# Optimization experiments

Hardware: AMD Instinct MI355X
Metric: run time of the kernel (lower is better)

## Reference

```python
import jax, jax.numpy as jnp
import numpy as np
from jax.scipy.special import logsumexp

B, S, E, H = 32, 1024, 512, 256  # batch, seq_len, sent_emb_dim, per-direction lstm hidden
NT, NTB = 16, 5
PAD, SOS, EOS = 0, 1, 2
NEG = -1000000.0


def _lstm(x, h0, c0, wih, whh, bih, bhh):
    # x: [B,S,I] -> outputs [B,S,H]; torch gate order i,f,g,o
    def step(carry, xt):
        h, c = carry
        z = xt @ wih.T + h @ whh.T + bih + bhh
        i, f, g, o = jnp.split(z, 4, axis=-1)
        c = jax.nn.sigmoid(f) * c + jax.nn.sigmoid(i) * jnp.tanh(g)
        h = jax.nn.sigmoid(o) * jnp.tanh(c)
        return (h, c), h
    _, hs = jax.lax.scan(step, (h0, c0), jnp.swapaxes(x, 0, 1))
    return jnp.swapaxes(hs, 0, 1)


def _bilstm(x, h0, c0, pf, pb):
    fwd = _lstm(x, h0[0], c0[0], *pf)
    bwd = _lstm(x[:, ::-1], h0[1], c0[1], *pb)[:, ::-1]
    return jnp.concatenate([fwd, bwd], axis=-1)  # [B,S,2H]


def _crf_nll(emissions, tags, mask, T):
    # gold-path score
    first = T[SOS, tags[:, 0]] + jnp.take_along_axis(emissions[:, 0], tags[:, 0:1], axis=1)[:, 0]
    e = jnp.take_along_axis(emissions, tags[:, :, None], axis=2)[:, :, 0]        # [B,S]
    tr = T[tags[:, :-1], tags[:, 1:]]                                            # [B,S-1]
    scores = first + jnp.sum((e[:, 1:] + tr) * mask[:, 1:], axis=1)
    last_idx = mask.sum(1).astype(jnp.int32) - 1
    last_tags = jnp.take_along_axis(tags, last_idx[:, None], axis=1)[:, 0]
    scores = scores + T[last_tags, EOS]
    # log partition via sequential DP (scan over time)
    alphas0 = T[SOS][None, :] + emissions[:, 0]
    es = jnp.swapaxes(emissions, 0, 1)[1:]   # [S-1,B,nt]
    ms = mask.T[1:]                          # [S-1,B]
    def step(alphas, inp):
        e_t, m_t = inp
        sc = e_t[:, None, :] + T[None, :, :] + alphas[:, :, None]  # [B,nt,nt]
        new = logsumexp(sc, axis=1)
        m = m_t[:, None]
        return m * new + (1.0 - m) * alphas, None
    alphas, _ = jax.lax.scan(step, alphas0, (es, ms))
    logZ = logsumexp(alphas + T[:, EOS][None, :], axis=1)
    return -jnp.sum(scores - logZ)


def _make_trans(key, nt):
    t = jax.random.uniform(key, (nt, nt), minval=-0.1, maxval=0.1)
    t = t.at[:, SOS].set(NEG).at[EOS, :].set(NEG)
    t = t.at[PAD, :].set(NEG).at[:, PAD].set(NEG)
    t = t.at[PAD, EOS].set(0.0).at[PAD, PAD].set(0.0)
    return t


def setup_inputs() -> dict:
    key = jax.random.key(0)
    ks = iter(jax.random.split(key, 40))
    sc = 0.05
    inp = {}
    inp['x'] = jax.random.normal(next(ks), (B, S, E), jnp.float32)
    inp['x_binary'] = jax.random.normal(next(ks), (B, S, 3 * E), jnp.float32)
    lengths = jax.random.randint(next(ks), (B,), S // 2, S + 1)
    inp['mask'] = (jnp.arange(S)[None, :] < lengths[:, None]).astype(jnp.float32)
    tg = jax.random.randint(next(ks), (B, S), 3, NT)
    inp['tags'] = jnp.where(inp['mask'] > 0, tg, PAD).astype(jnp.int32)
    tgb = jax.random.randint(next(ks), (B, S), 3, NTB)
    inp['tags_bin'] = jnp.where(inp['mask'] > 0, tgb, PAD).astype(jnp.int32)
    inp['trans'] = _make_trans(next(ks), NT)
    inp['trans_bin'] = _make_trans(next(ks), NTB)
    # binary emitter BiLSTM (input 3E)
    for nm, shp in [('w2f_ih', (4 * H, 3 * E)), ('w2f_hh', (4 * H, H)), ('b2f_ih', (4 * H,)), ('b2f_hh', (4 * H,)),
                    ('w2b_ih', (4 * H, 3 * E)), ('w2b_hh', (4 * H, H)), ('b2b_ih', (4 * H,)), ('b2b_hh', (4 * H,)),
                    ('w_bin', (NTB, 2 * H)), ('bb_bin', (NTB,)),
                    ('w1f_ih', (4 * H, E)), ('w1f_hh', (4 * H, H)), ('b1f_ih', (4 * H,)), ('b1f_hh', (4 * H,)),
                    ('w1b_ih', (4 * H, E)), ('w1b_hh', (4 * H, H)), ('b1b_ih', (4 * H,)), ('b1b_hh', (4 * H,)),
                    ('w_tag', (NT, 4 * H)), ('b_tag', (NT,))]:
        inp[nm] = jax.random.normal(next(ks), shp, jnp.float32) * sc
    inp['h0_bin'] = jax.random.normal(next(ks), (2, B, H), jnp.float32)
    inp['c0_bin'] = jax.random.normal(next(ks), (2, B, H), jnp.float32)
    inp['h0_main'] = jax.random.normal(next(ks), (2, B, H), jnp.float32)
    inp['c0_main'] = jax.random.normal(next(ks), (2, B, H), jnp.float32)
    return inp


def reference(x, x_binary, mask, tags, tags_bin, trans, trans_bin,
              w2f_ih, w2f_hh, b2f_ih, b2f_hh, w2b_ih, w2b_hh, b2b_ih, b2b_hh, w_bin, bb_bin, h0_bin, c0_bin,
              w1f_ih, w1f_hh, b1f_ih, b1f_hh, w1b_ih, w1b_hh, b1b_ih, b1b_hh, w_tag, b_tag, h0_main, c0_main):
    # binary branch: BiLSTM over 3E features -> hidden [B,S,2H] and 5-tag emissions
    hid_bin = _bilstm(x_binary, h0_bin, c0_bin,
                      (w2f_ih, w2f_hh, b2f_ih, b2f_hh), (w2b_ih, w2b_hh, b2b_ih, b2b_hh))
    emis_bin = hid_bin @ w_bin.T + bb_bin
    # main branch: BiLSTM over E features, concat with binary hidden -> n_tags emissions
    hid_main = _bilstm(x, h0_main, c0_main,
                       (w1f_ih, w1f_hh, b1f_ih, b1f_hh), (w1b_ih, w1b_hh, b1b_ih, b1b_hh))
    final = jnp.concatenate([hid_main, hid_bin], axis=-1)  # [B,S,4H] (dropout omitted: eval mode)
    emis = final @ w_tag.T + b_tag
    nll = _crf_nll(emis, tags, mask, trans)
    nll_bin = _crf_nll(emis_bin, tags_bin, mask, trans_bin)
    return jnp.stack([nll, nll_bin])
```

## Files before the change

### kernel.cpp

```cpp
#include <hip/hip_runtime.h>

typedef _Float16 f16;
typedef _Float16 f16x2 __attribute__((ext_vector_type(2)));
typedef _Float16 f16x4 __attribute__((ext_vector_type(4)));
typedef _Float16 f16x8 __attribute__((ext_vector_type(8)));
typedef float f32x4 __attribute__((ext_vector_type(4)));
typedef int iv4 __attribute__((ext_vector_type(4)));

#define S_LEN 1024
#define BATCH 32
#define HID 256
#define L2E 1.4426950408889634f
#define L2E2 2.8853900817779268f

#if __has_builtin(__builtin_amdgcn_fdot2)
#define FDOT2(a, b, c) __builtin_amdgcn_fdot2((a), (b), (c), false)
#else
static __device__ __forceinline__ float FDOT2(f16x2 a, f16x2 b, float c) {
  return c + (float)a[0] * (float)b[0] + (float)a[1] * (float)b[1];
}
#endif

__device__ __forceinline__ float EXP2(float x) {
#if __has_builtin(__builtin_amdgcn_exp2f)
  return __builtin_amdgcn_exp2f(x);
#else
  return exp2f(x);
#endif
}
__device__ __forceinline__ float RCP(float x) {
#if __has_builtin(__builtin_amdgcn_rcpf)
  return __builtin_amdgcn_rcpf(x);
#else
  return 1.0f / x;
#endif
}

__device__ __forceinline__ iv4 cvt8(float4 a, float4 b) {
#if __has_builtin(__builtin_amdgcn_cvt_pkrtz)
  auto p0 = __builtin_amdgcn_cvt_pkrtz(a.x, a.y);
  auto p1 = __builtin_amdgcn_cvt_pkrtz(a.z, a.w);
  auto p2 = __builtin_amdgcn_cvt_pkrtz(b.x, b.y);
  auto p3 = __builtin_amdgcn_cvt_pkrtz(b.z, b.w);
  iv4 o;
  o[0] = __builtin_bit_cast(int, p0);
  o[1] = __builtin_bit_cast(int, p1);
  o[2] = __builtin_bit_cast(int, p2);
  o[3] = __builtin_bit_cast(int, p3);
  return o;
#else
  f16x8 h;
  h[0] = (f16)a.x; h[1] = (f16)a.y; h[2] = (f16)a.z; h[3] = (f16)a.w;
  h[4] = (f16)b.x; h[5] = (f16)b.y; h[6] = (f16)b.z; h[7] = (f16)b.w;
  return __builtin_bit_cast(iv4, h);
#endif
}

#if __has_builtin(__builtin_amdgcn_global_load_lds)
__device__ __forceinline__ void gload16(const void* g, void* l) {
  __builtin_amdgcn_global_load_lds((const __attribute__((address_space(1))) void*)g,
                                   (__attribute__((address_space(3))) void*)l, 16, 0, 0);
}
#else
__device__ __forceinline__ void gload16(const void* g, void* l) {
  int lane = __builtin_amdgcn_mbcnt_hi(~0u, __builtin_amdgcn_mbcnt_lo(~0u, 0));
  ((f16x8*)l)[lane] = *(const f16x8*)g;
}
#endif

#define WG_BARRIER()                                                  \
  do {                                                                \
    __builtin_amdgcn_sched_barrier(0);                                \
    asm volatile("s_waitcnt lgkmcnt(0)\n\ts_barrier" ::: "memory");   \
    __builtin_amdgcn_sched_barrier(0);                                \
  } while (0)

__device__ __forceinline__ float dot8(f16x8 w, f16x8 h, float acc) {
  f16x2 a, b;
  a[0] = w[0]; a[1] = w[1]; b[0] = h[0]; b[1] = h[1]; acc = FDOT2(a, b, acc);
  a[0] = w[2]; a[1] = w[3]; b[0] = h[2]; b[1] = h[3]; acc = FDOT2(a, b, acc);
  a[0] = w[4]; a[1] = w[5]; b[0] = h[4]; b[1] = h[5]; acc = FDOT2(a, b, acc);
  a[0] = w[6]; a[1] = w[7]; b[0] = h[6]; b[1] = h[7]; acc = FDOT2(a, b, acc);
  return acc;
}

__global__ void cvt_f32_f16(const float* __restrict__ src, f16* __restrict__ dst, int n4) {
  int i = blockIdx.x * 256 + threadIdx.x;
  if (i < n4) {
    float4 v = ((const float4*)src)[i];
    f16x4 h;
    h[0] = (f16)v.x; h[1] = (f16)v.y; h[2] = (f16)v.z; h[3] = (f16)v.w;
    ((f16x4*)dst)[i] = h;
  }
}

__global__ void cvt_wih(const float* __restrict__ src, f16* __restrict__ dst, int K, int total8) {
  int i = blockIdx.x * 256 + threadIdx.x;
  if (i < total8) {
    int row = (int)(((long long)i * 8) / K);
    float sc = (row >= 512 && row < 768) ? L2E2 : L2E;
    const float* s = src + (size_t)i * 8;
    float4 a = *(const float4*)s;
    float4 b = *(const float4*)(s + 4);
    f16x8 h;
    h[0] = (f16)(a.x * sc); h[1] = (f16)(a.y * sc); h[2] = (f16)(a.z * sc); h[3] = (f16)(a.w * sc);
    h[4] = (f16)(b.x * sc); h[5] = (f16)(b.y * sc); h[6] = (f16)(b.z * sc); h[7] = (f16)(b.w * sc);
    *(f16x8*)(dst + (size_t)i * 8) = h;
  }
}

__global__ void bias_pack(const float* __restrict__ a0, const float* __restrict__ h0,
                          const float* __restrict__ a1, const float* __restrict__ h1,
                          const float* __restrict__ a2, const float* __restrict__ h2,
                          const float* __restrict__ a3, const float* __restrict__ h3,
                          float* __restrict__ bsum) {
  int i = blockIdx.x * 256 + threadIdx.x;
  if (i < 4096) {
    int u = i >> 10, n = i & 1023;
    float sc = (n >= 512 && n < 768) ? L2E2 : L2E;
    const float* pa = u == 0 ? a0 : u == 1 ? a1 : u == 2 ? a2 : a3;
    const float* ph = u == 0 ? h0 : u == 1 ? h1 : u == 2 ? h2 : h3;
    bsum[i] = (pa[n] + ph[n]) * sc;
  }
}

__global__ __launch_bounds__(256) void quant_whh(const float* __restrict__ src,
                                                 char* __restrict__ dstq,
                                                 float* __restrict__ fsc) {
  const int row = blockIdx.x * 4 + (threadIdx.x >> 6);
  const int lane = threadIdx.x & 63;
  const float sc = (row >= 512 && row < 768) ? L2E2 : L2E;
  float4 v = *(const float4*)(src + (size_t)row * 256 + lane * 4);
  float w0 = v.x * sc, w1 = v.y * sc, w2 = v.z * sc, w3 = v.w * sc;
  float mx = fmaxf(fmaxf(fabsf(w0), fabsf(w1)), fmaxf(fabsf(w2), fabsf(w3)));
#pragma unroll
  for (int off = 1; off < 64; off <<= 1) mx = fmaxf(mx, __shfl_xor(mx, off));
  mx = fmaxf(mx, 1e-20f);
  float inv = 127.0f / mx;
  int q0 = (int)rintf(w0 * inv), q1 = (int)rintf(w1 * inv);
  int q2 = (int)rintf(w2 * inv), q3 = (int)rintf(w3 * inv);
  int pk = (q0 & 0xff) | ((q1 & 0xff) << 8) | ((q2 & 0xff) << 16) | ((q3 & 0xff) << 24);
  ((int*)(dstq + (size_t)row * 256))[lane] = pk;
  if (lane == 0) fsc[row] = mx / 16129.0f;
}

__global__ __launch_bounds__(256) void proj_gemm(const float* __restrict__ x,
                                                 const float* __restrict__ xbin,
                                                 const f16* __restrict__ w16all,
                                                 const float* __restrict__ bsum,
                                                 char* __restrict__ P4) {
  __shared__ __align__(16) char smem[49152];
  const int L = blockIdx.x;
  const int q = L >> 5, r = L & 31;
  const int v = r >> 3;
  const int ub = q * 8 + (r & 7);
  const int unit = ub >> 8;
  const int bm = ub & 255;
  const int K = (unit < 2) ? 512 : 1536;
  const float* Aptr = (unit < 2) ? x : xbin;
  const size_t woff = (unit == 0) ? 0u : (unit == 1) ? 524288u : (unit == 2) ? 1048576u : 2621440u;
  const f16* W16 = w16all + woff;
  const int bgrp = bm >> 5, t0 = (bm & 31) * 32;
  const int b0 = bgrp * 4, c = bgrp >> 1, lkb = bgrp & 1;
  const int tid = threadIdx.x;
  const int lane = tid & 63, wid = tid >> 6;
  const int wm = wid >> 1, wn = wid & 1;
  const int lr = lane & 15, lk = lane >> 4;
  const int xsw = (lr & 7) << 4;

  f32x4 acc[4][8];
#pragma unroll
  for (int i = 0; i < 4; ++i)
#pragma unroll
    for (int n = 0; n < 8; ++n) acc[i][n] = (f32x4){0.f, 0.f, 0.f, 0.f};

  for (int k0 = 0; k0 < K; k0 += 64) {
#pragma unroll
    for (int i = 0; i < 8; ++i) {
      int g = (wid * 8 + i) * 64 + lane;
      int brow = g >> 3, cg = g & 7;
      const f16* bsrc = W16 + (size_t)(v * 256 + brow) * K + k0 + ((cg ^ (brow & 7)) << 3);
      gload16(bsrc, smem + 16384 + (wid * 8 + i) * 1024);
    }
#pragma unroll
    for (int s = 0; s < 4; ++s) {
      int slot = s * 256 + tid;
      int row = slot >> 3, seg = slot & 7;
      size_t arow = (size_t)(b0 + (row >> 5)) * 1024 + t0 + (row & 31);
      const float* ga = Aptr + arow * K + k0 + seg * 8;
      float4 v0 = *(const float4*)ga;
      float4 v1 = *(const float4*)(ga + 4);
      *(iv4*)(smem + row * 128 + ((seg ^ (row & 7)) << 4)) = cvt8(v0, v1);
    }
    __syncthreads();
#pragma unroll
    for (int kk = 0; kk < 2; ++kk) {
      f16x8 af[4], bf[8];
#pragma unroll
      for (int mi = 0; mi < 4; ++mi) {
        int ba = (wm * 64 + mi * 16 + lr) * 128 + kk * 64 + lk * 16;
        af[mi] = *(const f16x8*)(smem + (ba ^ xsw));
      }
#pragma unroll
      for (int ni = 0; ni < 8; ++ni) {
        int bb = (wn * 128 + ni * 16 + lr) * 128 + kk * 64 + lk * 16;
        bf[ni] = *(const f16x8*)(smem + 16384 + (bb ^ xsw));
      }
#pragma unroll
      for (int mi = 0; mi < 4; ++mi)
#pragma unroll
        for (int ni = 0; ni < 8; ++ni)
          acc[mi][ni] = __builtin_amdgcn_mfma_f32_16x16x32_f16(af[mi], bf[ni], acc[mi][ni], 0, 0, 0);
    }
    __syncthreads();
  }

  float biasv[8];
#pragma unroll
  for (int ni = 0; ni < 8; ++ni)
    biasv[ni] = bsum[unit * 1024 + v * 256 + wn * 128 + ni * 16 + lr];
  char* Pv = P4 + ((size_t)unit << 26) + ((size_t)v << 24);
#pragma unroll
  for (int pass = 0; pass < 2; ++pass) {
    __syncthreads();
#pragma unroll
    for (int mi2 = 0; mi2 < 2; ++mi2) {
      int mi = mi2 * 2 + pass;
#pragma unroll
      for (int ni = 0; ni < 8; ++ni) {
        int col = wn * 128 + ni * 16 + lr;
        int wc = col >> 5, jc = (col >> 4) & 1, lc = col & 15;
#pragma unroll
        for (int rr = 0; rr < 4; ++rr) {
          int row = wm * 64 + mi * 16 + lk * 4 + rr;
          int bsub = row >> 5, tl = row & 15;
          int unit2 = tl * 256 + wc * 32 + jc * 16 + lc;
          int off = (unit2 * 8 + bsub * 2) ^ ((tl & 7) << 4);
          *(f16*)(smem + off) = (f16)(acc[mi][ni][rr] + biasv[ni]);
        }
      }
    }
    __syncthreads();
#pragma unroll
    for (int k = 0; k < 16; ++k) {
      int uid = k * 256 + tid;
      int tl = uid >> 8, sub = uid & 255;
      int off = (uid * 8) ^ ((tl & 7) << 4);
      unsigned long long val = *(const unsigned long long*)(smem + off);
      int t_loc = pass * 16 + tl;
      int wq = sub >> 5, jq = (sub >> 4) & 1, lq = sub & 15;
      size_t didx =
          (((size_t)((t0 + t_loc) * 4 + c) * 512) + wq * 64 + jq * 32 + lkb * 16 + lq) << 3;
      *(unsigned long long*)(Pv + didx) = val;
    }
  }
}

__global__ __attribute__((amdgpu_flat_work_group_size(512, 512), amdgpu_waves_per_eu(2, 2)))
void lstm_rec5(const char* __restrict__ Wq4,
               const float* __restrict__ fsc4,
               const char* __restrict__ P4,
               const float* __restrict__ h0m,
               const float* __restrict__ c0m,
               const float* __restrict__ h0b,
               const float* __restrict__ c0b,
               f16* __restrict__ hid4) {
  const int wg = blockIdx.x;
  const int u = wg >> 4, c16 = wg & 15;
  const int dir = u & 1;
  const int tid = threadIdx.x;
  const int l = tid & 63, w = tid >> 6;
  const int lr = l & 15, lk = l >> 4;
  const int jj = lk >> 1, selb = lk & 1;
  const int r2 = lr & 1;
  const int swzA = r2 ? 80 : 0;
  const int swzW = selb ? 80 : 0;
  const int j = w * 32 + jj * 16 + lr;

  __shared__ __align__(16) char hbuf[2][512];

  iv4 Bf[4][8];
  const char* wb = Wq4 + ((size_t)u << 18);
#pragma unroll
  for (int nt = 0; nt < 8; ++nt) {
    int n = (nt >> 1) * 256 + w * 32 + ((nt & 1) << 4) + lr;
#pragma unroll
    for (int ks = 0; ks < 4; ++ks)
      Bf[ks][nt] = *(const iv4*)(wb + (size_t)n * 256 + ks * 64 + lk * 16);
  }
  float fv[4], fv4[4];
#pragma unroll
  for (int v = 0; v < 4; ++v) {
    fv[v] = fsc4[u * 1024 + v * 256 + j];
    fv4[v] = fv[v] * 4.f;
  }

  const int b = c16 * 2 + selb;
  const float* h0 = (u < 2 ? h0m : h0b) + (size_t)dir * BATCH * HID;
  const float* c0 = (u < 2 ? c0m : c0b) + (size_t)dir * BATCH * HID;
  float cst = c0[b * HID + j];
  {
    float hv = h0[b * HID + j] * 31.75f;
    int hq = (int)rintf(hv);
    hq = hq > 127 ? 127 : (hq < -127 ? -127 : hq);
    hbuf[0][selb * 256 + (j ^ swzW)] = (char)hq;
  }

  const char* Pc = P4 + ((size_t)u << 26);
  const size_t soff =
      (size_t)((w * 64 + jj * 32 + (((c16 >> 1) & 1) << 4) + lr) * 8 + (c16 & 1) * 4);
  const int cq = c16 >> 2;
  f16x2 Pa[4], Pb[4];
  {
    int t0 = dir ? (S_LEN - 1) : 0;
    size_t tb = ((size_t)((t0 << 2) + cq) << 12) + soff;
#pragma unroll
    for (int v = 0; v < 4; ++v) Pa[v] = *(const f16x2*)(Pc + ((size_t)v << 24) + tb);
  }
  WG_BARRIER();

#define LSTM_STEP(S_, SP_, PC_, PN_, FV_)                                                   \
  {                                                                                         \
    const int t = dir ? (S_LEN - 1 - (S_)) : (S_);                                          \
    {                                                                                       \
      int s2 = ((S_) + 1 < S_LEN) ? (S_) + 1 : (S_);                                        \
      int t2 = dir ? (S_LEN - 1 - s2) : s2;                                                 \
      size_t tb = ((size_t)((t2 << 2) + cq) << 12) + soff;                                  \
      _Pragma("unroll") for (int v = 0; v < 4; ++v)                                         \
          PN_[v] = *(const f16x2*)(Pc + ((size_t)v << 24) + tb);                            \
    }                                                                                       \
    iv4 ia[8];                                                                              \
    _Pragma("unroll") for (int nt = 0; nt < 8; ++nt) ia[nt] = (iv4){0, 0, 0, 0};            \
    const char* hb = hbuf[SP_];                                                             \
    _Pragma("unroll") for (int ks = 0; ks < 4; ++ks) {                                      \
      iv4 Af = *(const iv4*)(hb + r2 * 256 + ((ks * 64 + lk * 16) ^ swzA));                 \
      _Pragma("unroll") for (int nt = 0; nt < 8; ++nt)                                      \
          ia[nt] = __builtin_amdgcn_mfma_i32_16x16x64_i8(Af, Bf[ks][nt], ia[nt], 0, 0, 0);  \
    }                                                                                       \
    float z[4];                                                                             \
    _Pragma("unroll") for (int v = 0; v < 4; ++v) {                                         \
      int e0 = selb ? ia[v * 2][1] : ia[v * 2][0];                                          \
      int e1 = selb ? ia[v * 2 + 1][1] : ia[v * 2 + 1][0];                                  \
      int iz = jj ? e1 : e0;                                                                \
      float pv = selb ? (float)PC_[v][1] : (float)PC_[v][0];                                \
      z[v] = pv + FV_[v] * (float)iz;                                                       \
    }                                                                                       \
    float zi = z[0], zf = z[1], zg = z[2], zo = z[3];                                       \
    float ei = EXP2(-zi), ef = EXP2(-zf), eg = EXP2(-zg), eo = EXP2(-zo);                   \
    float di = 1.f + ei, df = 1.f + ef, dg = 1.f + eg, dof = 1.f + eo;                      \
    float r1 = RCP(di * df);                                                                \
    float si = r1 * df, sf = r1 * di;                                                       \
    float r2x = RCP(dg * dof);                                                              \
    float tg = 2.f * (r2x * dof) - 1.f, so = r2x * dg;                                      \
    float cc = sf * cst + si * tg;                                                          \
    cst = cc;                                                                               \
    float ec = EXP2(-L2E2 * cc);                                                            \
    float th = 2.f * RCP(1.f + ec) - 1.f;                                                   \
    float hh = so * th;                                                                     \
    int hq = (int)rintf(hh * 127.f);                                                        \
    hbuf[SP_ ^ 1][selb * 256 + (j ^ swzW)] = (char)hq;                                      \
    hid4[((size_t)b << 20) + ((size_t)t << 10) + (u << 8) + j] = (f16)hh;                   \
    WG_BARRIER();                                                                           \
  }

  LSTM_STEP(0, 0, Pa, Pb, fv4);
  for (int s = 1; s <= 1021; s += 2) {
    LSTM_STEP(s, 1, Pb, Pa, fv);
    LSTM_STEP(s + 1, 0, Pa, Pb, fv);
  }
  LSTM_STEP(1023, 1, Pb, Pa, fv);
#undef LSTM_STEP
}

__global__ __launch_bounds__(256) void emis_kernel(const f16* __restrict__ hid4,
                                                   const f16* __restrict__ wtag,
                                                   const float* __restrict__ btag,
                                                   const f16* __restrict__ wbin,
                                                   const float* __restrict__ bbin,
                                                   float* __restrict__ emis,
                                                   float* __restrict__ emisb) {
  const int tid = threadIdx.x;
  const int rl = tid >> 4, n = tid & 15;
  const size_t row = (size_t)blockIdx.x * 16 + rl;
  const f16x8* hv = (const f16x8*)(hid4 + row * 1024);
  const f16x8* wv = (const f16x8*)(wtag + n * 1024);
  float acc = btag[n];
#pragma unroll 8
  for (int kc = 0; kc < 128; ++kc) acc = dot8(wv[kc], hv[kc], acc);
  emis[row * 16 + n] = acc;
  if (n < 5) {
    const f16x8* hv2 = (const f16x8*)(hid4 + row * 1024 + 512);
    const f16x8* wv2 = (const f16x8*)(wbin + (size_t)n * 512);
    float a2 = bbin[n];
#pragma unroll 8
    for (int kc = 0; kc < 64; ++kc) a2 = dot8(wv2[kc], hv2[kc], a2);
    emisb[row * 5 + n] = a2;
  }
}

__global__ __launch_bounds__(64) void crf_logz(const float* __restrict__ emis,
                                               const float* __restrict__ trans,
                                               const float* __restrict__ emisb,
                                               const float* __restrict__ transb,
                                               const float* __restrict__ mask,
                                               float* __restrict__ outLogZ) {
  const int crf = blockIdx.x >> 5, b = blockIdx.x & 31;
  const int NTc = crf ? 5 : 16;
  const float* __restrict__ E = crf ? emisb : emis;
  const float* __restrict__ T = crf ? transb : trans;
  const int lane = threadIdx.x;
  const int jn = lane >> 2, p = lane & 3;
  const bool jv = (jn < NTc);
  const int jc = jv ? jn : 0;
  float Tc[4];
#pragma unroll
  for (int ii = 0; ii < 4; ++ii) {
    int i = p * 4 + ii;
    Tc[ii] = (jv && i < NTc) ? T[i * NTc + jn] : -1e30f;
  }
  __shared__ float as_[2][16];
  if (lane < 16) { as_[0][lane] = -1e30f; as_[1][lane] = -1e30f; }
  __syncthreads();
  float alpha = 0.f;
  if (jv && p == 0) {
    alpha = T[1 * NTc + jn] + E[(size_t)(b << 10) * NTc + jn];
    as_[0][jn] = alpha;
  }
  __syncthreads();
  int cur = 0;
  const size_t ebase = (size_t)(b << 10) * NTc + jc;
  const int mbase = b << 10;
#define LDE(tt) E[ebase + (size_t)(tt)*NTc]
#define LDM(tt) mask[mbase + (tt)]

  auto step = [&](float e_tj, float m_t) {
    float v0 = (jv && (p * 4 + 0) < NTc) ? (as_[cur][p * 4 + 0] + Tc[0]) : -1e30f;
    float v1 = (jv && (p * 4 + 1) < NTc) ? (as_[cur][p * 4 + 1] + Tc[1]) : -1e30f;
    float v2 = (jv && (p * 4 + 2) < NTc) ? (as_[cur][p * 4 + 2] + Tc[2]) : -1e30f;
    float v3 = (jv && (p * 4 + 3) < NTc) ? (as_[cur][p * 4 + 3] + Tc[3]) : -1e30f;
    float mx = fmaxf(fmaxf(v0, v1), fmaxf(v2, v3));
    mx = fmaxf(mx, __shfl_xor(mx, 1, 4));
    mx = fmaxf(mx, __shfl_xor(mx, 2, 4));
    float ss = __expf(v0 - mx) + __expf(v1 - mx) + __expf(v2 - mx) + __expf(v3 - mx);
    ss += __shfl_xor(ss, 1, 4);
    ss += __shfl_xor(ss, 2, 4);
    if (jv && p == 0) {
      float newv = e_tj + mx + __logf(ss);
      alpha = (m_t > 0.5f) ? newv : alpha;
      as_[cur ^ 1][jn] = alpha;
    }
    __syncthreads();
    cur ^= 1;
  };

  float eb[4], mb[4];
#pragma unroll
  for (int k = 0; k < 4; ++k) { eb[k] = LDE(1 + k); mb[k] = LDM(1 + k); }
  for (int t = 1; t <= 1017; t += 4) {
    float en[4], mn[4];
#pragma unroll
    for (int k = 0; k < 4; ++k) {
      int ix = t + 4 + k;
      ix = ix > 1023 ? 1023 : ix;
      en[k] = LDE(ix);
      mn[k] = LDM(ix);
    }
    step(eb[0], mb[0]); step(eb[1], mb[1]); step(eb[2], mb[2]); step(eb[3], mb[3]);
#pragma unroll
    for (int k = 0; k < 4; ++k) { eb[k] = en[k]; mb[k] = mn[k]; }
  }
  step(eb[0], mb[0]); step(eb[1], mb[1]); step(eb[2], mb[2]);
#undef LDE
#undef LDM

  if (lane == 0) {
    float mx = -1e30f;
    for (int jjx = 0; jjx < NTc; ++jjx) mx = fmaxf(mx, as_[cur][jjx] + T[jjx * NTc + 2]);
    float ss = 0.f;
    for (int jjx = 0; jjx < NTc; ++jjx) ss += __expf(as_[cur][jjx] + T[jjx * NTc + 2] - mx);
    outLogZ[crf * 32 + b] = mx + __logf(ss);
  }
}

__global__ __launch_bounds__(64) void crf_score(const float* __restrict__ emis,
                                                const float* __restrict__ trans,
                                                const float* __restrict__ emisb,
                                                const float* __restrict__ transb,
                                                const float* __restrict__ mask,
                                                const int* __restrict__ tags,
                                                const int* __restrict__ tagsb,
                                                float* __restrict__ outScore) {
  const int crf = blockIdx.x >> 5, b = blockIdx.x & 31;
  const int NTc = crf ? 5 : 16;
  const float* __restrict__ E = crf ? emisb : emis;
  const float* __restrict__ T = crf ? transb : trans;
  const int* __restrict__ tg = (crf ? tagsb : tags) + (b << 10);
  const float* __restrict__ mk = mask + (b << 10);
  const int lane = threadIdx.x;
  float s = 0.f, cnt = 0.f;
  for (int t = lane; t < S_LEN; t += 64) {
    float m = mk[t];
    cnt += m;
    if (t >= 1 && m > 0.5f)
      s += E[((size_t)(b << 10) + t) * NTc + tg[t]] + T[tg[t - 1] * NTc + tg[t]];
  }
#pragma unroll
  for (int off = 32; off >= 1; off >>= 1) {
    s += __shfl_down(s, off);
    cnt += __shfl_down(cnt, off);
  }
  if (lane == 0) {
    int L = (int)(cnt + 0.5f);
    int t0 = tg[0];
    float tot = T[1 * NTc + t0] + E[(size_t)(b << 10) * NTc + t0] + s + T[tg[L - 1] * NTc + 2];
    outScore[crf * 32 + b] = tot;
  }
}

__global__ void finalk(const float* __restrict__ logZ, const float* __restrict__ score,
                       float* __restrict__ out) {
  int j = threadIdx.x;
  if (j < 2) {
    float a = 0.f;
    for (int b = 0; b < 32; ++b) a += logZ[j * 32 + b] - score[j * 32 + b];
    out[j] = a;
  }
}

extern "C" void kernel_launch(void* const* d_in, const int* in_sizes, int n_in,
                              void* d_out, int out_size, void* d_ws, size_t ws_size,
                              hipStream_t stream) {
  const float* x       = (const float*)d_in[0];
  const float* xbin    = (const float*)d_in[1];
  const float* mask    = (const float*)d_in[2];
  const int*   tags    = (const int*)d_in[3];
  const int*   tagsb   = (const int*)d_in[4];
  const float* trans   = (const float*)d_in[5];
  const float* transb  = (const float*)d_in[6];
  const float* w2f_ih  = (const float*)d_in[7];
  const float* w2f_hh  = (const float*)d_in[8];
  const float* b2f_ih  = (const float*)d_in[9];
  const float* b2f_hh  = (const float*)d_in[10];
  const float* w2b_ih  = (const float*)d_in[11];
  const float* w2b_hh  = (const float*)d_in[12];
  const float* b2b_ih  = (const float*)d_in[13];
  const float* b2b_hh  = (const float*)d_in[14];
  const float* w_bin   = (const float*)d_in[15];
  const float* bb_bin  = (const float*)d_in[16];
  const float* w1f_ih  = (const float*)d_in[17];
  const float* w1f_hh  = (const float*)d_in[18];
  const float* b1f_ih  = (const float*)d_in[19];
  const float* b1f_hh  = (const float*)d_in[20];
  const float* w1b_ih  = (const float*)d_in[21];
  const float* w1b_hh  = (const float*)d_in[22];
  const float* b1b_ih  = (const float*)d_in[23];
  const float* b1b_hh  = (const float*)d_in[24];
  const float* w_tag   = (const float*)d_in[25];
  const float* b_tag   = (const float*)d_in[26];
  const float* h0_bin  = (const float*)d_in[27];
  const float* c0_bin  = (const float*)d_in[28];
  const float* h0_main = (const float*)d_in[29];
  const float* c0_main = (const float*)d_in[30];

  char* ws = (char*)d_ws;
  char* P4    = ws;
  f16* hid4   = (f16*)(ws + 268435456);
  char* Wq4   = ws + 335544320;
  float* fsc4 = (float*)(ws + 336592896);
  f16* wtag   = (f16*)(ws + 336609280);
  f16* wbin   = (f16*)(ws + 336642048);
  float* emis  = (float*)(ws + 336647168);
  float* emisb = (float*)(ws + 338744320);
  float* logZ  = (float*)(ws + 339399680);
  float* score = (float*)(ws + 339399936);
  float* bsum  = (float*)(ws + 339400704);
  f16* w16all  = (f16*)(ws + 340000768);

  quant_whh<<<256, 256, 0, stream>>>(w1f_hh, Wq4 + 0 * 262144, fsc4 + 0 * 1024);
  quant_whh<<<256, 256, 0, stream>>>(w1b_hh, Wq4 + 1 * 262144, fsc4 + 1 * 1024);
  quant_whh<<<256, 256, 0, stream>>>(w2f_hh, Wq4 + 2 * 262144, fsc4 + 2 * 1024);
  quant_whh<<<256, 256, 0, stream>>>(w2b_hh, Wq4 + 3 * 262144, fsc4 + 3 * 1024);
  cvt_f32_f16<<<16, 256, 0, stream>>>(w_tag, wtag, 4096);
  cvt_f32_f16<<<3, 256, 0, stream>>>(w_bin, wbin, 640);
  cvt_wih<<<256, 256, 0, stream>>>(w1f_ih, w16all + 0, 512, 65536);
  cvt_wih<<<256, 256, 0, stream>>>(w1b_ih, w16all + 524288, 512, 65536);
  cvt_wih<<<768, 256, 0, stream>>>(w2f_ih, w16all + 1048576, 1536, 196608);
  cvt_wih<<<768, 256, 0, stream>>>(w2b_ih, w16all + 2621440, 1536, 196608);
  bias_pack<<<16, 256, 0, stream>>>(b1f_ih, b1f_hh, b1b_ih, b1b_hh,
                                    b2f_ih, b2f_hh, b2b_ih, b2b_hh, bsum);

  proj_gemm<<<4096, 256, 0, stream>>>(x, xbin, w16all, bsum, P4);

  lstm_rec5<<<64, 512, 0, stream>>>(Wq4, fsc4, P4, h0_main, c0_main, h0_bin, c0_bin, hid4);
  emis_kernel<<<2048, 256, 0, stream>>>(hid4, wtag, b_tag, wbin, bb_bin, emis, emisb);
  crf_logz<<<64, 64, 0, stream>>>(emis, trans, emisb, transb, mask, logZ);
  crf_score<<<64, 64, 0, stream>>>(emis, trans, emisb, transb, mask, tags, tagsb, score);
  finalk<<<1, 64, 0, stream>>>(logZ, score, (float*)d_out);
}
```

Baseline: 1.988 ms.

## Pre-convert activations to fp16 and use async LDS loads in projection GEMM

Adds a pass that converts x and x_binary to fp16 in workspace, so the projection GEMM can stage its A tiles with direct global-to-LDS loads instead of fp32 loads, register conversion and LDS stores. This path is taken only when the workspace is large enough. Separately, the CRF logZ kernel, which runs as a single wave, replaces its workgroup barriers with an LDS wait only. The cost is an extra read and write pass over the inputs before the GEMM, and the barrier removal depends on the block being exactly one wave.

```diff
diff --git a/kernel.cpp b/kernel.cpp
--- a/kernel.cpp
+++ b/kernel.cpp
@@ -75,6 +75,13 @@
     __builtin_amdgcn_sched_barrier(0);                                \
   } while (0)
 
+#define WAVE_SYNC()                                                   \
+  do {                                                                \
+    __builtin_amdgcn_sched_barrier(0);                                \
+    asm volatile("s_waitcnt lgkmcnt(0)" ::: "memory");                \
+    __builtin_amdgcn_sched_barrier(0);                                \
+  } while (0)
+
 __device__ __forceinline__ float dot8(f16x8 w, f16x8 h, float acc) {
   f16x2 a, b;
   a[0] = w[0]; a[1] = w[1]; b[0] = h[0]; b[1] = h[1]; acc = FDOT2(a, b, acc);
@@ -91,6 +98,16 @@
     f16x4 h;
     h[0] = (f16)v.x; h[1] = (f16)v.y; h[2] = (f16)v.z; h[3] = (f16)v.w;
     ((f16x4*)dst)[i] = h;
+  }
+}
+
+__global__ void cvt_x16(const float* __restrict__ src, f16* __restrict__ dst, int n8) {
+  int i = blockIdx.x * 256 + threadIdx.x;
+  if (i < n8) {
+    const float* s = src + (size_t)i * 8;
+    float4 a = *(const float4*)s;
+    float4 b = *(const float4*)(s + 4);
+    *(iv4*)(dst + (size_t)i * 8) = cvt8(a, b);
   }
 }
 
@@ -144,8 +161,11 @@
   if (lane == 0) fsc[row] = mx / 16129.0f;
 }
 
+template <bool PRE>
 __global__ __launch_bounds__(256) void proj_gemm(const float* __restrict__ x,
                                                  const float* __restrict__ xbin,
+                                                 const f16* __restrict__ x16,
+                                                 const f16* __restrict__ xbin16,
                                                  const f16* __restrict__ w16all,
                                                  const float* __restrict__ bsum,
                                                  char* __restrict__ P4) {
@@ -158,6 +178,7 @@
   const int bm = ub & 255;
   const int K = (unit < 2) ? 512 : 1536;
   const float* Aptr = (unit < 2) ? x : xbin;
+  const f16* A16 = (unit < 2) ? x16 : xbin16;
   const size_t woff = (unit == 0) ? 0u : (unit == 1) ? 524288u : (unit == 2) ? 1048576u : 2621440u;
   const f16* W16 = w16all + woff;
   const int bgrp = bm >> 5, t0 = (bm & 31) * 32;
@@ -182,15 +203,27 @@
       const f16* bsrc = W16 + (size_t)(v * 256 + brow) * K + k0 + ((cg ^ (brow & 7)) << 3);
       gload16(bsrc, smem + 16384 + (wid * 8 + i) * 1024);
     }
-#pragma unroll
-    for (int s = 0; s < 4; ++s) {
-      int slot = s * 256 + tid;
-      int row = slot >> 3, seg = slot & 7;
-      size_t arow = (size_t)(b0 + (row >> 5)) * 1024 + t0 + (row & 31);
-      const float* ga = Aptr + arow * K + k0 + seg * 8;
-      float4 v0 = *(const float4*)ga;
-      float4 v1 = *(const float4*)(ga + 4);
-      *(iv4*)(smem + row * 128 + ((seg ^ (row & 7)) << 4)) = cvt8(v0, v1);
+    if constexpr (PRE) {
+#pragma unroll
+      for (int s = 0; s < 4; ++s) {
+        int g = s * 256 + tid;
+        int row = g >> 3, pos = g & 7;
+        int seg = pos ^ (row & 7);
+        size_t arow = (size_t)(b0 + (row >> 5)) * 1024 + t0 + (row & 31);
+        const f16* asrc = A16 + arow * K + k0 + seg * 8;
+        gload16(asrc, smem + (s * 256 + (tid >> 6) * 64) * 16 + (tid & 63) * 16);
+      }
+    } else {
+#pragma unroll
+      for (int s = 0; s < 4; ++s) {
+        int slot = s * 256 + tid;
+        int row = slot >> 3, seg = slot & 7;
+        size_t arow = (size_t)(b0 + (row >> 5)) * 1024 + t0 + (row & 31);
+        const float* ga = Aptr + arow * K + k0 + seg * 8;
+        float4 v0 = *(const float4*)ga;
+        float4 v1 = *(const float4*)(ga + 4);
+        *(iv4*)(smem + row * 128 + ((seg ^ (row & 7)) << 4)) = cvt8(v0, v1);
+      }
     }
     __syncthreads();
 #pragma unroll
@@ -420,13 +453,13 @@
   }
   __shared__ float as_[2][16];
   if (lane < 16) { as_[0][lane] = -1e30f; as_[1][lane] = -1e30f; }
-  __syncthreads();
+  WAVE_SYNC();
   float alpha = 0.f;
   if (jv && p == 0) {
     alpha = T[1 * NTc + jn] + E[(size_t)(b << 10) * NTc + jn];
     as_[0][jn] = alpha;
   }
-  __syncthreads();
+  WAVE_SYNC();
   int cur = 0;
   const size_t ebase = (size_t)(b << 10) * NTc + jc;
   const int mbase = b << 10;
@@ -449,7 +482,7 @@
       alpha = (m_t > 0.5f) ? newv : alpha;
       as_[cur ^ 1][jn] = alpha;
     }
-    __syncthreads();
+    WAVE_SYNC();
     cur ^= 1;
   };
 
@@ -575,6 +608,9 @@
   float* score = (float*)(ws + 339399936);
   float* bsum  = (float*)(ws + 339400704);
   f16* w16all  = (f16*)(ws + 340000768);
+  f16* x16     = (f16*)(ws + 348389376);
+  f16* xbin16  = (f16*)(ws + 381943808);
+  const bool pre = (ws_size >= 482607104ULL);
 
   quant_whh<<<256, 256, 0, stream>>>(w1f_hh, Wq4 + 0 * 262144, fsc4 + 0 * 1024);
   quant_whh<<<256, 256, 0, stream>>>(w1b_hh, Wq4 + 1 * 262144, fsc4 + 1 * 1024);
@@ -589,7 +625,13 @@
   bias_pack<<<16, 256, 0, stream>>>(b1f_ih, b1f_hh, b1b_ih, b1b_hh,
                                     b2f_ih, b2f_hh, b2b_ih, b2b_hh, bsum);
 
-  proj_gemm<<<4096, 256, 0, stream>>>(x, xbin, w16all, bsum, P4);
+  if (pre) {
+    cvt_x16<<<8192, 256, 0, stream>>>(x, x16, 2097152);
+    cvt_x16<<<24576, 256, 0, stream>>>(xbin, xbin16, 6291456);
+    proj_gemm<true><<<4096, 256, 0, stream>>>(x, xbin, x16, xbin16, w16all, bsum, P4);
+  } else {
+    proj_gemm<false><<<4096, 256, 0, stream>>>(x, xbin, x16, xbin16, w16all, bsum, P4);
+  }
 
   lstm_rec5<<<64, 512, 0, stream>>>(Wq4, fsc4, P4, h0_main, c0_main, h0_bin, c0_bin, hid4);
   emis_kernel<<<2048, 256, 0, stream>>>(hid4, wtag, b_tag, wbin, bb_bin, emis, emisb);
```

New measurement: 1.968 ms. About the same (-1.0%).

## Double-buffer projection GEMM tiles and use wave-level sync in CRF forward

Applied to the files above, without the earlier changes.

The input projection GEMM now uses two LDS stages. The next K-slice of A is prefetched into registers and B is loaded into LDS with global_load_lds while the current slice feeds the MFMAs, so global load latency overlaps compute. This doubles shared memory to 96KB, which may reduce occupancy. The CRF log-partition kernel runs as a single wave, so its per-timestep __syncthreads is replaced by an LDS waitcnt only, removing barrier overhead from the sequential 1023-step loop.

```diff
diff --git a/kernel.cpp b/kernel.cpp
--- a/kernel.cpp
+++ b/kernel.cpp
@@ -75,6 +75,13 @@
     __builtin_amdgcn_sched_barrier(0);                                \
   } while (0)
 
+#define WAVE_SYNC()                                                   \
+  do {                                                                \
+    __builtin_amdgcn_sched_barrier(0);                                \
+    asm volatile("s_waitcnt lgkmcnt(0)" ::: "memory");                \
+    __builtin_amdgcn_sched_barrier(0);                                \
+  } while (0)
+
 __device__ __forceinline__ float dot8(f16x8 w, f16x8 h, float acc) {
   f16x2 a, b;
   a[0] = w[0]; a[1] = w[1]; b[0] = h[0]; b[1] = h[1]; acc = FDOT2(a, b, acc);
@@ -149,7 +156,7 @@
                                                  const f16* __restrict__ w16all,
                                                  const float* __restrict__ bsum,
                                                  char* __restrict__ P4) {
-  __shared__ __align__(16) char smem[49152];
+  __shared__ __align__(16) char smem[98304];
   const int L = blockIdx.x;
   const int q = L >> 5, r = L & 31;
   const int v = r >> 3;
@@ -174,46 +181,66 @@
 #pragma unroll
     for (int n = 0; n < 8; ++n) acc[i][n] = (f32x4){0.f, 0.f, 0.f, 0.f};
 
-  for (int k0 = 0; k0 < K; k0 += 64) {
-#pragma unroll
-    for (int i = 0; i < 8; ++i) {
-      int g = (wid * 8 + i) * 64 + lane;
-      int brow = g >> 3, cg = g & 7;
-      const f16* bsrc = W16 + (size_t)(v * 256 + brow) * K + k0 + ((cg ^ (brow & 7)) << 3);
-      gload16(bsrc, smem + 16384 + (wid * 8 + i) * 1024);
-    }
-#pragma unroll
-    for (int s = 0; s < 4; ++s) {
-      int slot = s * 256 + tid;
-      int row = slot >> 3, seg = slot & 7;
-      size_t arow = (size_t)(b0 + (row >> 5)) * 1024 + t0 + (row & 31);
-      const float* ga = Aptr + arow * K + k0 + seg * 8;
-      float4 v0 = *(const float4*)ga;
-      float4 v1 = *(const float4*)(ga + 4);
-      *(iv4*)(smem + row * 128 + ((seg ^ (row & 7)) << 4)) = cvt8(v0, v1);
-    }
-    __syncthreads();
-#pragma unroll
-    for (int kk = 0; kk < 2; ++kk) {
-      f16x8 af[4], bf[8];
-#pragma unroll
-      for (int mi = 0; mi < 4; ++mi) {
-        int ba = (wm * 64 + mi * 16 + lr) * 128 + kk * 64 + lk * 16;
-        af[mi] = *(const f16x8*)(smem + (ba ^ xsw));
-      }
-#pragma unroll
-      for (int ni = 0; ni < 8; ++ni) {
-        int bb = (wn * 128 + ni * 16 + lr) * 128 + kk * 64 + lk * 16;
-        bf[ni] = *(const f16x8*)(smem + 16384 + (bb ^ xsw));
-      }
-#pragma unroll
-      for (int mi = 0; mi < 4; ++mi)
-#pragma unroll
-        for (int ni = 0; ni < 8; ++ni)
-          acc[mi][ni] = __builtin_amdgcn_mfma_f32_16x16x32_f16(af[mi], bf[ni], acc[mi][ni], 0, 0, 0);
-    }
-    __syncthreads();
-  }
+#define PROJ_PREFETCH(KN_, AO_, BO_)                                                        \
+  if ((KN_) < K) {                                                                          \
+    float4 ar0[4], ar1[4];                                                                  \
+    _Pragma("unroll") for (int s = 0; s < 4; ++s) {                                         \
+      int slot = s * 256 + tid;                                                             \
+      int row = slot >> 3, seg = slot & 7;                                                  \
+      size_t arow = (size_t)(b0 + (row >> 5)) * 1024 + t0 + (row & 31);                     \
+      const float* ga = Aptr + arow * K + (KN_) + seg * 8;                                  \
+      ar0[s] = *(const float4*)ga;                                                          \
+      ar1[s] = *(const float4*)(ga + 4);                                                    \
+    }                                                                                       \
+    __builtin_amdgcn_sched_barrier(0);                                                      \
+    _Pragma("unroll") for (int i = 0; i < 8; ++i) {                                         \
+      int g = (wid * 8 + i) * 64 + lane;                                                    \
+      int brow = g >> 3, cg = g & 7;                                                        \
+      const f16* bsrc = W16 + (size_t)(v * 256 + brow) * K + (KN_) + ((cg ^ (brow & 7)) << 3); \
+      gload16(bsrc, smem + (BO_) + (wid * 8 + i) * 1024);                                   \
+    }                                                                                       \
+    __builtin_amdgcn_sched_barrier(0);                                                      \
+    _Pragma("unroll") for (int s = 0; s < 4; ++s) {                                         \
+      int slot = s * 256 + tid;                                                             \
+      int row = slot >> 3, seg = slot & 7;                                                  \
+      *(iv4*)(smem + (AO_) + row * 128 + ((seg ^ (row & 7)) << 4)) = cvt8(ar0[s], ar1[s]);  \
+    }                                                                                       \
+    __builtin_amdgcn_sched_barrier(0);                                                      \
+  } else {                                                                                  \
+    __builtin_amdgcn_sched_barrier(0);                                                      \
+    asm volatile("s_waitcnt vmcnt(0)" ::: "memory");                                        \
+    __builtin_amdgcn_sched_barrier(0);                                                      \
+  }
+
+#define PROJ_COMPUTE(AO_, BO_)                                                              \
+  _Pragma("unroll") for (int kk = 0; kk < 2; ++kk) {                                        \
+    f16x8 af[4], bf[8];                                                                     \
+    _Pragma("unroll") for (int mi = 0; mi < 4; ++mi) {                                      \
+      int ba = (wm * 64 + mi * 16 + lr) * 128 + kk * 64 + lk * 16;                          \
+      af[mi] = *(const f16x8*)(smem + (AO_) + (ba ^ xsw));                                  \
+    }                                                                                       \
+    _Pragma("unroll") for (int ni = 0; ni < 8; ++ni) {                                      \
+      int bb = (wn * 128 + ni * 16 + lr) * 128 + kk * 64 + lk * 16;                         \
+      bf[ni] = *(const f16x8*)(smem + (BO_) + (bb ^ xsw));                                  \
+    }                                                                                       \
+    _Pragma("unroll") for (int mi = 0; mi < 4; ++mi)                                        \
+      _Pragma("unroll") for (int ni = 0; ni < 8; ++ni)                                      \
+        acc[mi][ni] = __builtin_amdgcn_mfma_f32_16x16x32_f16(af[mi], bf[ni], acc[mi][ni], 0, 0, 0); \
+  }
+
+  PROJ_PREFETCH(0, 0, 32768);
+  for (int k0 = 0; k0 < K; k0 += 128) {
+    PROJ_PREFETCH(k0 + 64, 16384, 65536);
+    WG_BARRIER();
+    PROJ_COMPUTE(0, 32768);
+    WG_BARRIER();
+    PROJ_PREFETCH(k0 + 128, 0, 32768);
+    WG_BARRIER();
+    PROJ_COMPUTE(16384, 65536);
+    WG_BARRIER();
+  }
+#undef PROJ_PREFETCH
+#undef PROJ_COMPUTE
 
   float biasv[8];
 #pragma unroll
@@ -420,13 +447,13 @@
   }
   __shared__ float as_[2][16];
   if (lane < 16) { as_[0][lane] = -1e30f; as_[1][lane] = -1e30f; }
-  __syncthreads();
+  WAVE_SYNC();
   float alpha = 0.f;
   if (jv && p == 0) {
     alpha = T[1 * NTc + jn] + E[(size_t)(b << 10) * NTc + jn];
     as_[0][jn] = alpha;
   }
-  __syncthreads();
+  WAVE_SYNC();
   int cur = 0;
   const size_t ebase = (size_t)(b << 10) * NTc + jc;
   const int mbase = b << 10;
@@ -449,7 +476,7 @@
       alpha = (m_t > 0.5f) ? newv : alpha;
       as_[cur ^ 1][jn] = alpha;
     }
-    __syncthreads();
+    WAVE_SYNC();
     cur ^= 1;
   };
 
```

After: 1.959 ms. No clear change (-1.5%).
